# Kernel tuning notes

Hardware: AMD Instinct MI355X
Metric: run time of the kernel (lower is better)

Reference implementation:

```python
import jax, jax.numpy as jnp
import numpy as np

# Config matching init_kwargs: layer_nb=1 -> stride 16, image 608x608 -> 38x38 grid
B, CIN, H, W = 32, 512, 38, 38
NA, NC = 3, 80
STRIDE = 16.0
ANCHORS = np.array([[30.0, 61.0], [62.0, 45.0], [59.0, 119.0]], dtype=np.float32)


def setup_inputs() -> dict:
    key = jax.random.key(0)
    k1, k2, k3 = jax.random.split(key, 3)
    xin = jax.random.normal(k1, (B, CIN, H, W), dtype=jnp.float32)
    # 1x1 conv weight stored as (out_ch, in_ch); out_ch = NA*(NC+5) = 255
    conv_w = jax.random.normal(k2, (NA * (NC + 5), CIN), dtype=jnp.float32) * 0.02
    conv_b = jax.random.normal(k3, (NA * (NC + 5),), dtype=jnp.float32) * 0.01
    return {"xin": xin, "conv_w": conv_w, "conv_b": conv_b}


def reference(xin, conv_w, conv_b):
    # 1x1 conv == channel GEMM; fuse the NCHW->NHWC permute into the einsum
    fm = jnp.einsum('bchw,oc->bhwo', xin, conv_w) + conv_b  # [B,H,W,255]
    fm = fm.reshape(B, H, W, NA, NC + 5)
    tx, ty, tw, th = fm[..., 0], fm[..., 1], fm[..., 2], fm[..., 3]
    # grid offsets (precomputed via broadcasting instead of per-call numpy rebuild)
    x_off = jnp.arange(W, dtype=fm.dtype)[None, None, :, None]   # broadcast over B,H,NA
    y_off = jnp.arange(H, dtype=fm.dtype)[None, :, None, None]   # broadcast over B,W,NA
    anchors = jnp.asarray(ANCHORS, dtype=fm.dtype)               # [NA,2]
    bx = (jax.nn.sigmoid(tx) + x_off) * STRIDE
    by = (jax.nn.sigmoid(ty) + y_off) * STRIDE
    bw = jnp.exp(tw) * anchors[:, 0]
    bh = jnp.exp(th) * anchors[:, 1]
    boxes = jnp.stack([bx, by, bw, bh], axis=-1)                 # [B,H,W,NA,4]
    # concat decoded boxes with raw objectness + class logits -> [B,H,W,NA,85]
    return jnp.concatenate([boxes, fm[..., 4:]], axis=-1)
```

## Files before the change

kernel.cpp:

```cpp
#include <hip/hip_runtime.h>
#include <cstdint>
#include <cstddef>

#define CIN_K  512
#define WW_    38
#define BHW    1444
#define NOUT   255
#define MTOT   46208

#define ROW_E  520
#define ROW_DW 260

typedef __attribute__((ext_vector_type(8))) short  bf16x8;
typedef __attribute__((ext_vector_type(4))) float  floatx4;

static __device__ __forceinline__ unsigned f2bf(float f) {
    unsigned u = __builtin_bit_cast(unsigned, f);
    return (u + 0x7FFFu + ((u >> 16) & 1u)) >> 16;
}

__global__ void conv_w_to_bf16(const float* __restrict__ cw,
                               unsigned short* __restrict__ wb) {
    int tg   = blockIdx.x * 256 + threadIdx.x;
    int base = tg * 8;
    int n    = base >> 9;
    unsigned rr[4] = {0u, 0u, 0u, 0u};
    if (n < NOUT) {
        float4 v0 = *(const float4*)(cw + base);
        float4 v1 = *(const float4*)(cw + base + 4);
        rr[0] = f2bf(v0.x) | (f2bf(v0.y) << 16);
        rr[1] = f2bf(v0.z) | (f2bf(v0.w) << 16);
        rr[2] = f2bf(v1.x) | (f2bf(v1.y) << 16);
        rr[3] = f2bf(v1.z) | (f2bf(v1.w) << 16);
    }
    *(uint4*)(wb + base) = *(uint4*)rr;
}

__global__ __launch_bounds__(256, 2)
void yolo_head(const float* __restrict__ xin,
               const unsigned short* __restrict__ wb,
               const float* __restrict__ cb,
               float* __restrict__ out)
{
    __shared__ unsigned int smem[64 * ROW_DW];
    unsigned short* As = (unsigned short*)smem;

    const int t    = threadIdx.x;
    const int w    = t >> 6;
    const int lane = t & 63;
    const int l15  = lane & 15;
    const int q    = lane >> 4;
    const int m0   = blockIdx.x * 64;

    {
        const int mloc = lane;
        int m  = m0 + mloc;
        int bi = m / BHW;
        int hw = m - bi * BHW;
        const float* pa = xin + (size_t)bi * (CIN_K * BHW) + hw;
#pragma unroll
        for (int s = 0; s < 16; ++s) {
            const int k0 = s * 32 + w * 8;
            float v[8];
#pragma unroll
            for (int u = 0; u < 8; ++u) v[u] = pa[(size_t)(k0 + u) * BHW];
            unsigned pk[4];
#pragma unroll
            for (int u2 = 0; u2 < 4; ++u2)
                pk[u2] = f2bf(v[2 * u2]) | (f2bf(v[2 * u2 + 1]) << 16);
            *(uint4*)(&As[mloc * ROW_E + k0]) = *(uint4*)pk;
        }
    }
    __syncthreads();

    floatx4 acc[4][4];
#pragma unroll
    for (int i = 0; i < 4; ++i)
#pragma unroll
        for (int j = 0; j < 4; ++j)
            acc[i][j] = (floatx4){0.f, 0.f, 0.f, 0.f};

    const unsigned short* pbw = wb + (size_t)(w * 64 + l15) * CIN_K + q * 8;

#pragma unroll
    for (int kc = 0; kc < 16; ++kc) {
        bf16x8 bfr[4], af[4];
#pragma unroll
        for (int j = 0; j < 4; ++j) {
            uint4 bv = *(const uint4*)(pbw + (size_t)j * 16 * CIN_K + kc * 32);
            bfr[j] = __builtin_bit_cast(bf16x8, bv);
        }
#pragma unroll
        for (int i = 0; i < 4; ++i) {
            int4 av = *(const int4*)(&As[(i * 16 + l15) * ROW_E + kc * 32 + q * 8]);
            af[i] = __builtin_bit_cast(bf16x8, av);
        }
#pragma unroll
        for (int i = 0; i < 4; ++i)
#pragma unroll
            for (int j = 0; j < 4; ++j)
                acc[i][j] = __builtin_amdgcn_mfma_f32_16x16x32_bf16(
                                af[i], bfr[j], acc[i][j], 0, 0, 0);
    }

#pragma unroll
    for (int j = 0; j < 4; ++j) {
        int   n    = w * 64 + j * 16 + l15;
        int   nc   = n < NOUT ? n : NOUT - 1;
        int   ai   = nc / 85;
        int   ji   = nc - ai * 85;
        float bias = cb[nc];
        float aw   = (ai == 0) ? 30.f : (ai == 1) ? 62.f : 59.f;
        float ah   = (ai == 0) ? 61.f : (ai == 1) ? 45.f : 119.f;
#pragma unroll
        for (int i = 0; i < 4; ++i)
#pragma unroll
            for (int r = 0; r < 4; ++r) {
                int   md  = m0 + i * 16 + q * 4 + r;
                int   rem = md % BHW;
                int   hh  = rem / WW_;
                float v   = acc[i][j][r] + bias;
                float res;
                if (ji == 0)      res = (1.f / (1.f + __expf(-v)) + (float)(rem - hh * WW_)) * 16.f;
                else if (ji == 1) res = (1.f / (1.f + __expf(-v)) + (float)hh) * 16.f;
                else if (ji == 2) res = __expf(v) * aw;
                else if (ji == 3) res = __expf(v) * ah;
                else              res = v;
                acc[i][j][r] = res;
            }
    }

    __syncthreads();
    float* EP = (float*)smem;

#pragma unroll
    for (int i = 0; i < 4; ++i)
#pragma unroll
        for (int j = 0; j < 4; ++j)
#pragma unroll
            for (int r = 0; r < 4; ++r)
                EP[(i * 16 + q * 4 + r) * ROW_DW + w * 64 + j * 16 + l15] = acc[i][j][r];

    __syncthreads();

    {
        float*       ob  = out + (size_t)(m0 + w * 16) * NOUT;
        const float* EPb = (const float*)smem + (w * 16) * ROW_DW;
#pragma unroll
        for (int s2 = 0; s2 < 16; ++s2) {
            int f4 = s2 * 64 + lane;
            if (f4 < 1020) {
                int   f = f4 * 4;
                float vv[4];
#pragma unroll
                for (int e = 0; e < 4; ++e) {
                    int fe = f + e;
                    int mr = fe / NOUT;
                    int x  = fe - mr * NOUT;
                    vv[e]  = EPb[mr * ROW_DW + x];
                }
                *(float4*)(ob + f) = make_float4(vv[0], vv[1], vv[2], vv[3]);
            }
        }
    }
}

extern "C" void kernel_launch(void* const* d_in, const int* in_sizes, int n_in,
                              void* d_out, int out_size, void* d_ws, size_t ws_size,
                              hipStream_t stream) {
    const float* xin = (const float*)d_in[0];
    const float* cw  = (const float*)d_in[1];
    const float* cb  = (const float*)d_in[2];
    float*       out = (float*)d_out;
    unsigned short* wb = (unsigned short*)d_ws;

    hipLaunchKernelGGL(conv_w_to_bf16, dim3(64), dim3(256), 0, stream, cw, wb);
    hipLaunchKernelGGL(yolo_head, dim3(MTOT / 64), dim3(256), 0, stream,
                       xin, wb, cb, out);
}
```

Measured before the change: 195.2 us.

## Split K staging into two LDS chunks to double occupancy, vectorize input loads

Activation tiles are now staged in shared memory in two K halves of 256 instead of all 512 at once. The epilogue writes its transpose buffer in two 32-row passes, which halves the shared memory per block and lets the launch bound rise from 2 to 4 blocks per CU. Each thread now reads float4 vectors covering 4 pixels by 4 channels and packs them to bf16, replacing scalar strided loads. The cost is extra barriers between chunks and passes, and more register pressure under the tighter launch bound.

```diff
diff --git a/kernel.cpp b/kernel.cpp
--- a/kernel.cpp
+++ b/kernel.cpp
@@ -8,8 +8,9 @@
 #define NOUT   255
 #define MTOT   46208
 
-#define ROW_E  520
-#define ROW_DW 260
+#define KCH    256
+#define ROW_E  260
+#define EP_DW  260
 
 typedef __attribute__((ext_vector_type(8))) short  bf16x8;
 typedef __attribute__((ext_vector_type(4))) float  floatx4;
@@ -36,13 +37,13 @@
     *(uint4*)(wb + base) = *(uint4*)rr;
 }
 
-__global__ __launch_bounds__(256, 2)
+__global__ __launch_bounds__(256, 4)
 void yolo_head(const float* __restrict__ xin,
                const unsigned short* __restrict__ wb,
                const float* __restrict__ cb,
                float* __restrict__ out)
 {
-    __shared__ unsigned int smem[64 * ROW_DW];
+    __shared__ unsigned smem[64 * (ROW_E / 2)];
     unsigned short* As = (unsigned short*)smem;
 
     const int t    = threadIdx.x;
@@ -52,26 +53,12 @@
     const int q    = lane >> 4;
     const int m0   = blockIdx.x * 64;
 
-    {
-        const int mloc = lane;
-        int m  = m0 + mloc;
-        int bi = m / BHW;
-        int hw = m - bi * BHW;
-        const float* pa = xin + (size_t)bi * (CIN_K * BHW) + hw;
-#pragma unroll
-        for (int s = 0; s < 16; ++s) {
-            const int k0 = s * 32 + w * 8;
-            float v[8];
-#pragma unroll
-            for (int u = 0; u < 8; ++u) v[u] = pa[(size_t)(k0 + u) * BHW];
-            unsigned pk[4];
-#pragma unroll
-            for (int u2 = 0; u2 < 4; ++u2)
-                pk[u2] = f2bf(v[2 * u2]) | (f2bf(v[2 * u2 + 1]) << 16);
-            *(uint4*)(&As[mloc * ROW_E + k0]) = *(uint4*)pk;
-        }
-    }
-    __syncthreads();
+    const int mq4 = (t & 15) * 4;
+    const int kq4 = (t >> 4) * 4;
+    const int m4  = m0 + mq4;
+    const int bi  = m4 / BHW;
+    const int hw  = m4 - bi * BHW;
+    const float* pb0 = xin + (size_t)bi * (CIN_K * BHW) + hw;
 
     floatx4 acc[4][4];
 #pragma unroll
@@ -83,24 +70,48 @@
     const unsigned short* pbw = wb + (size_t)(w * 64 + l15) * CIN_K + q * 8;
 
 #pragma unroll
-    for (int kc = 0; kc < 16; ++kc) {
-        bf16x8 bfr[4], af[4];
+    for (int ck = 0; ck < 2; ++ck) {
+        if (ck) __syncthreads();
+
 #pragma unroll
-        for (int j = 0; j < 4; ++j) {
-            uint4 bv = *(const uint4*)(pbw + (size_t)j * 16 * CIN_K + kc * 32);
-            bfr[j] = __builtin_bit_cast(bf16x8, bv);
+        for (int it = 0; it < 4; ++it) {
+            const int kl = it * 64 + kq4;
+            alignas(16) float vv[4][4];
+#pragma unroll
+            for (int kk = 0; kk < 4; ++kk)
+                *(float4*)&vv[kk][0] =
+                    *(const float4*)(pb0 + (size_t)(ck * KCH + kl + kk) * BHW);
+#pragma unroll
+            for (int r = 0; r < 4; ++r) {
+                unsigned lo = f2bf(vv[0][r]) | (f2bf(vv[1][r]) << 16);
+                unsigned hi = f2bf(vv[2][r]) | (f2bf(vv[3][r]) << 16);
+                uint2 pk = make_uint2(lo, hi);
+                *(uint2*)(&As[(mq4 + r) * ROW_E + kl]) = pk;
+            }
         }
+        __syncthreads();
+
 #pragma unroll
-        for (int i = 0; i < 4; ++i) {
-            int4 av = *(const int4*)(&As[(i * 16 + l15) * ROW_E + kc * 32 + q * 8]);
-            af[i] = __builtin_bit_cast(bf16x8, av);
+        for (int kc = 0; kc < 8; ++kc) {
+            bf16x8 bfr[4], af[4];
+#pragma unroll
+            for (int j = 0; j < 4; ++j) {
+                uint4 bv = *(const uint4*)(pbw + (size_t)j * 16 * CIN_K
+                                           + ck * KCH + kc * 32);
+                bfr[j] = __builtin_bit_cast(bf16x8, bv);
+            }
+#pragma unroll
+            for (int i = 0; i < 4; ++i) {
+                int4 av = *(const int4*)(&As[(i * 16 + l15) * ROW_E + kc * 32 + q * 8]);
+                af[i] = __builtin_bit_cast(bf16x8, av);
+            }
+#pragma unroll
+            for (int i = 0; i < 4; ++i)
+#pragma unroll
+                for (int j = 0; j < 4; ++j)
+                    acc[i][j] = __builtin_amdgcn_mfma_f32_16x16x32_bf16(
+                                    af[i], bfr[j], acc[i][j], 0, 0, 0);
         }
-#pragma unroll
-        for (int i = 0; i < 4; ++i)
-#pragma unroll
-            for (int j = 0; j < 4; ++j)
-                acc[i][j] = __builtin_amdgcn_mfma_f32_16x16x32_bf16(
-                                af[i], bfr[j], acc[i][j], 0, 0, 0);
     }
 
 #pragma unroll
@@ -130,36 +141,38 @@
             }
     }
 
-    __syncthreads();
     float* EP = (float*)smem;
+#pragma unroll
+    for (int p = 0; p < 2; ++p) {
+        __syncthreads();
+#pragma unroll
+        for (int i2 = 0; i2 < 2; ++i2) {
+            const int i = p * 2 + i2;
+#pragma unroll
+            for (int j = 0; j < 4; ++j)
+#pragma unroll
+                for (int r = 0; r < 4; ++r)
+                    EP[(i2 * 16 + q * 4 + r) * EP_DW + w * 64 + j * 16 + l15] =
+                        acc[i][j][r];
+        }
+        __syncthreads();
 
+        const float* EPb = (const float*)smem + (w * 8) * EP_DW;
+        float*       ob  = out + (size_t)(m0 + p * 32 + w * 8) * NOUT;
 #pragma unroll
-    for (int i = 0; i < 4; ++i)
-#pragma unroll
-        for (int j = 0; j < 4; ++j)
-#pragma unroll
-            for (int r = 0; r < 4; ++r)
-                EP[(i * 16 + q * 4 + r) * ROW_DW + w * 64 + j * 16 + l15] = acc[i][j][r];
-
-    __syncthreads();
-
-    {
-        float*       ob  = out + (size_t)(m0 + w * 16) * NOUT;
-        const float* EPb = (const float*)smem + (w * 16) * ROW_DW;
-#pragma unroll
-        for (int s2 = 0; s2 < 16; ++s2) {
+        for (int s2 = 0; s2 < 8; ++s2) {
             int f4 = s2 * 64 + lane;
-            if (f4 < 1020) {
+            if (f4 < 510) {
                 int   f = f4 * 4;
-                float vv[4];
+                float vs[4];
 #pragma unroll
                 for (int e = 0; e < 4; ++e) {
                     int fe = f + e;
                     int mr = fe / NOUT;
                     int x  = fe - mr * NOUT;
-                    vv[e]  = EPb[mr * ROW_DW + x];
+                    vs[e]  = EPb[mr * EP_DW + x];
                 }
-                *(float4*)(ob + f) = make_float4(vv[0], vv[1], vv[2], vv[3]);
+                *(float4*)(ob + f) = make_float4(vs[0], vs[1], vs[2], vs[3]);
             }
         }
     }
```

New measurement: 181.3 us. 7.1% less time.
